# Optimization experiments

Measured on AMD Instinct MI355X. Metric: run time of the kernel, lower is better.

Reference implementation:

```python
import jax, jax.numpy as jnp
import numpy as np

ALPHA = 0.2  # leaky_relu negative slope


def setup_inputs() -> dict:
    key = jax.random.key(0)
    ks = jax.random.split(key, 6)
    N, E, F_IN, F_OUT, E_DIM = 50000, 800000, 256, 256, 64
    h = jax.random.normal(ks[0], (N, F_IN), dtype=jnp.float32)
    e_feat = jax.random.normal(ks[1], (E, E_DIM), dtype=jnp.float32)
    W = jax.random.normal(ks[2], (F_OUT, F_IN), dtype=jnp.float32) * (1.0 / np.sqrt(F_IN))
    A = jax.random.normal(ks[3], (1, 2 * F_OUT + E_DIM), dtype=jnp.float32) * 0.05
    src = jax.random.randint(ks[4], (E,), 0, N, dtype=jnp.int32)
    dst = jax.random.randint(ks[5], (E,), 0, N, dtype=jnp.int32)
    return {"h": h, "e_feat": e_feat, "W": W, "A": A, "src": src, "dst": dst}


def reference(h, e_feat, W, A, src, dst):
    N = h.shape[0]
    F_OUT = W.shape[0]
    # equation (1): node projection
    z = h @ W.T  # [N, F_OUT]
    z_src = z[src]  # [E, F_OUT]
    z_dst = z[dst]  # [E, F_OUT]
    # equation (2): per-edge attention logit = attn_fc([z_src, z_dst, e_feat])
    # split A to avoid materializing the [E, 2F+De] concat
    a_src, a_dst, a_e = A[0, :F_OUT], A[0, F_OUT:2 * F_OUT], A[0, 2 * F_OUT:]
    logits = z_src @ a_src + z_dst @ a_dst + e_feat @ a_e  # [E]
    e = jax.nn.leaky_relu(logits, ALPHA)
    # equations (3)&(4): segment-softmax over incoming edges per destination
    m = jax.ops.segment_max(e, dst, num_segments=N)  # [N]
    ex = jnp.exp(e - m[dst])
    denom = jax.ops.segment_sum(ex, dst, num_segments=N)  # [N]
    alpha = ex / denom[dst]  # [E]
    h_out = jax.ops.segment_sum(alpha[:, None] * z_src, dst, num_segments=N)
    return h_out
```

## Files before the change

### kernel.cpp

```cpp
#include <hip/hip_runtime.h>
#include <hip/hip_bf16.h>

#define FDIM 256
#define EDIM 64
#define LEAKY 0.2f

#define BM 128
#define BN 128
#define BK 32

typedef __attribute__((ext_vector_type(8))) short bfrag;
typedef __attribute__((ext_vector_type(4))) float f4acc;

__device__ __forceinline__ unsigned f2bf(float x){
    unsigned u = __float_as_uint(x);
    return (u + 0x7FFFu + ((u >> 16) & 1u)) >> 16;
}
__device__ __forceinline__ float bf2f(unsigned b){
    return __uint_as_float(b << 16);
}
__device__ __forceinline__ unsigned pack_hi(float x, float y, float& hx, float& hy){
    unsigned bx = f2bf(x), by = f2bf(y);
    hx = bf2f(bx); hy = bf2f(by);
    return bx | (by << 16);
}
__device__ __forceinline__ unsigned pack_lo(float rx, float ry){
    return f2bf(rx) | (f2bf(ry) << 16);
}

__global__ void k_init(float* __restrict__ s_src, float* __restrict__ s_dst,
                       int* __restrict__ counts, int N){
    int i = blockIdx.x*256 + threadIdx.x;
    if (i < N){ s_src[i] = 0.f; s_dst[i] = 0.f; counts[i] = 0; }
}

__global__ __launch_bounds__(256, 2) void k_gemm(const float* __restrict__ h,
                                                 const float* __restrict__ W,
                                                 const float* __restrict__ A,
                                                 unsigned short* __restrict__ z16,
                                                 float* __restrict__ s_src,
                                                 float* __restrict__ s_dst, int M){
    __shared__ uint4 smA[BM*8];
    __shared__ uint4 smB[BN*8];
    __shared__ float sred[2][2][BM];

    int tid = threadIdx.x;
    int m0 = blockIdx.x * BM;
    int n0 = blockIdx.y * BN;

    int wid  = tid >> 6;
    int lane = tid & 63;
    int wm = (wid >> 1) * 64;
    int wn = (wid & 1) * 64;
    int l15 = lane & 15;
    int l4  = lane >> 4;

    f4acc acc[4][4];
    #pragma unroll
    for (int i = 0; i < 4; ++i)
        #pragma unroll
        for (int j = 0; j < 4; ++j)
            acc[i][j] = (f4acc)(0.f);

    for (int kc = 0; kc < FDIM; kc += BK){
        #pragma unroll
        for (int q = 0; q < 4; ++q){
            int p = tid + q*256;
            int isB = p >= 512;
            int pp = p & 511;
            int row = pp >> 2, k8 = pp & 3;
            float4 v0, v1;
            if (isB){
                const float* g = &W[(n0 + row)*FDIM + kc + k8*8];
                v0 = *(const float4*)g; v1 = *(const float4*)(g + 4);
            } else {
                int gr = m0 + row;
                if (gr < M){
                    const float* g = &h[(size_t)gr*FDIM + kc + k8*8];
                    v0 = *(const float4*)g; v1 = *(const float4*)(g + 4);
                } else {
                    v0 = make_float4(0.f,0.f,0.f,0.f); v1 = v0;
                }
            }
            int sh = k8 ^ (row & 7);
            if (isB){
                uint4 hi; float hx, hy;
                hi.x = pack_hi(v0.x, v0.y, hx, hy);
                hi.y = pack_hi(v0.z, v0.w, hx, hy);
                hi.z = pack_hi(v1.x, v1.y, hx, hy);
                hi.w = pack_hi(v1.z, v1.w, hx, hy);
                smB[row*8 + sh] = hi;
            } else {
                uint4 hi, lo; float hx, hy;
                hi.x = pack_hi(v0.x, v0.y, hx, hy);
                lo.x = pack_lo(v0.x - hx, v0.y - hy);
                hi.y = pack_hi(v0.z, v0.w, hx, hy);
                lo.y = pack_lo(v0.z - hx, v0.w - hy);
                hi.z = pack_hi(v1.x, v1.y, hx, hy);
                lo.z = pack_lo(v1.x - hx, v1.y - hy);
                hi.w = pack_hi(v1.z, v1.w, hx, hy);
                lo.w = pack_lo(v1.z - hx, v1.w - hy);
                smA[row*8 + sh]       = hi;
                smA[row*8 + (sh ^ 4)] = lo;
            }
        }
        __syncthreads();

        bfrag ah[4], al[4];
        #pragma unroll
        for (int mf = 0; mf < 4; ++mf){
            int row = wm + mf*16 + l15;
            int sh = l4 ^ (row & 7);
            ah[mf] = *(const bfrag*)&smA[row*8 + sh];
            al[mf] = *(const bfrag*)&smA[row*8 + (sh ^ 4)];
        }
        #pragma unroll
        for (int nf = 0; nf < 4; ++nf){
            int row = wn + nf*16 + l15;
            int sh = l4 ^ (row & 7);
            bfrag bh = *(const bfrag*)&smB[row*8 + sh];
            #pragma unroll
            for (int mf = 0; mf < 4; ++mf){
                acc[mf][nf] = __builtin_amdgcn_mfma_f32_16x16x32_bf16(ah[mf], bh, acc[mf][nf], 0, 0, 0);
                acc[mf][nf] = __builtin_amdgcn_mfma_f32_16x16x32_bf16(al[mf], bh, acc[mf][nf], 0, 0, 0);
            }
        }
        __syncthreads();
    }

    #pragma unroll
    for (int mf = 0; mf < 4; ++mf){
        #pragma unroll
        for (int nf = 0; nf < 4; ++nf){
            int gcol = n0 + wn + nf*16 + l15;
            #pragma unroll
            for (int r = 0; r < 4; ++r){
                int grow = m0 + wm + mf*16 + l4*4 + r;
                if (grow < M)
                    z16[(size_t)grow*FDIM + gcol] = (unsigned short)f2bf(acc[mf][nf][r]);
            }
        }
    }

    float aS[4], aD[4];
    #pragma unroll
    for (int nf = 0; nf < 4; ++nf){
        int gcol = n0 + wn + nf*16 + l15;
        aS[nf] = A[gcol];
        aD[nf] = A[FDIM + gcol];
    }
    #pragma unroll
    for (int mf = 0; mf < 4; ++mf){
        #pragma unroll
        for (int r = 0; r < 4; ++r){
            float ps = 0.f, pd = 0.f;
            #pragma unroll
            for (int nf = 0; nf < 4; ++nf){
                ps += acc[mf][nf][r] * aS[nf];
                pd += acc[mf][nf][r] * aD[nf];
            }
            #pragma unroll
            for (int o = 1; o < 16; o <<= 1){
                ps += __shfl_xor(ps, o);
                pd += __shfl_xor(pd, o);
            }
            if (l15 == 0){
                int row = wm + mf*16 + l4*4 + r;
                sred[wid & 1][0][row] = ps;
                sred[wid & 1][1][row] = pd;
            }
        }
    }
    __syncthreads();
    if (tid < BM){
        int grow = m0 + tid;
        if (grow < M){
            atomicAdd(&s_src[grow], sred[0][0][tid] + sred[1][0][tid]);
            atomicAdd(&s_dst[grow], sred[0][1][tid] + sred[1][1][tid]);
        }
    }
}

__global__ void k_count(const int* __restrict__ dst, int* __restrict__ counts, int E){
    int e = blockIdx.x*256 + threadIdx.x;
    if (e < E) atomicAdd(&counts[dst[e]], 1);
}

__global__ void k_chunk_sums(const int* __restrict__ counts, int* __restrict__ bsums, int N){
    __shared__ int sh[256];
    int base = blockIdx.x*1024;
    int s = 0;
    for (int i = threadIdx.x; i < 1024; i += 256){
        int idx = base + i;
        s += (idx < N) ? counts[idx] : 0;
    }
    sh[threadIdx.x] = s; __syncthreads();
    for (int o = 128; o > 0; o >>= 1){
        if (threadIdx.x < o) sh[threadIdx.x] += sh[threadIdx.x + o];
        __syncthreads();
    }
    if (threadIdx.x == 0) bsums[blockIdx.x] = sh[0];
}

__global__ void k_scan_small(int* __restrict__ b, int nb){
    __shared__ int sh[1024];
    int tid = threadIdx.x;
    int v = (tid < nb) ? b[tid] : 0;
    sh[tid] = v; __syncthreads();
    int acc = v;
    for (int o = 1; o < 1024; o <<= 1){
        int t = (tid >= o) ? sh[tid - o] : 0;
        __syncthreads();
        acc += t; sh[tid] = acc;
        __syncthreads();
    }
    if (tid < nb) b[tid] = acc - v;
}

__global__ void k_scan_chunks(int* __restrict__ counts, int* __restrict__ cursor,
                              const int* __restrict__ bsums, int N, int E){
    __shared__ int sh[256];
    int tid = threadIdx.x;
    int base = blockIdx.x*1024 + tid*4;
    int v[4]; int s = 0;
    #pragma unroll
    for (int l = 0; l < 4; l++){
        int idx = base + l;
        v[l] = (idx < N) ? counts[idx] : 0;
        s += v[l];
    }
    sh[tid] = s; __syncthreads();
    int acc = s;
    for (int o = 1; o < 256; o <<= 1){
        int t = (tid >= o) ? sh[tid - o] : 0;
        __syncthreads();
        acc += t; sh[tid] = acc;
        __syncthreads();
    }
    int excl = acc - s + bsums[blockIdx.x];
    #pragma unroll
    for (int l = 0; l < 4; l++){
        int idx = base + l;
        if (idx < N){ counts[idx] = excl; cursor[idx] = excl; }
        excl += v[l];
    }
    if (blockIdx.x == 0 && tid == 0) counts[N] = E;
}

__global__ void k_edge(const float* __restrict__ ef, const float* __restrict__ A,
                       const float* __restrict__ s_src, const float* __restrict__ s_dst,
                       const int* __restrict__ src, const int* __restrict__ dst,
                       int* __restrict__ cursor, int2* __restrict__ epair, int E){
    int gt = blockIdx.x*256 + threadIdx.x;
    int e = gt >> 4, l4 = gt & 15;
    if (e >= E) return;
    float4 f  = *(const float4*)&ef[(size_t)e*EDIM + l4*4];
    float4 ae = *(const float4*)&A[2*FDIM + l4*4];
    float v = f.x*ae.x + f.y*ae.y + f.z*ae.z + f.w*ae.w;
    v += __shfl_xor(v, 8); v += __shfl_xor(v, 4);
    v += __shfl_xor(v, 2); v += __shfl_xor(v, 1);
    if (l4 == 0){
        int d = dst[e];
        float lg = v + s_src[src[e]] + s_dst[d];
        lg = lg > 0.f ? lg : LEAKY*lg;
        int p = atomicAdd(&cursor[d], 1);
        int2 pr; pr.x = src[e]; pr.y = __float_as_int(lg);
        epair[p] = pr;
    }
}

__global__ __launch_bounds__(256) void k_out(const unsigned short* __restrict__ z16,
                                             const int* __restrict__ offsets,
                                             const int2* __restrict__ epair,
                                             float* __restrict__ out, int N){
    int n = blockIdx.x*4 + (threadIdx.x >> 6);
    int lane = threadIdx.x & 63;
    if (n >= N) return;
    int i0 = offsets[n], i1 = offsets[n+1];

    float mlane = -3.402823466e38f;
    for (int i = i0 + lane; i < i1; i += 64)
        mlane = fmaxf(mlane, __int_as_float(epair[i].y));
    float mx = mlane;
    #pragma unroll
    for (int o = 32; o > 0; o >>= 1)
        mx = fmaxf(mx, __shfl_xor(mx, o));

    float4 a[4];
    a[0] = make_float4(0,0,0,0); a[1] = a[0]; a[2] = a[0]; a[3] = a[0];
    float dw = 0.f;
    const unsigned short* zb = z16 + lane*4;

    for (int base = i0; base < i1; base += 64){
        int cnt = min(64, i1 - base);
        int2 pe = make_int2(0, 0);
        float w = 0.f;
        if (lane < cnt){
            pe = epair[base + lane];
            w = __expf(__int_as_float(pe.y) - mx);
        }
        dw += w;
        int j = 0;
        for (; j + 7 < cnt; j += 8){
            float wj[8]; int sj[8]; uint2 rj[8];
            #pragma unroll
            for (int q = 0; q < 8; ++q){
                wj[q] = __shfl(w, j + q);
                sj[q] = __shfl(pe.x, j + q);
            }
            #pragma unroll
            for (int q = 0; q < 8; ++q)
                rj[q] = *(const uint2*)&zb[(size_t)sj[q]*FDIM];
            #pragma unroll
            for (int q = 0; q < 8; ++q){
                a[q & 3].x += wj[q]*bf2f(rj[q].x & 0xffffu);
                a[q & 3].y += wj[q]*bf2f(rj[q].x >> 16);
                a[q & 3].z += wj[q]*bf2f(rj[q].y & 0xffffu);
                a[q & 3].w += wj[q]*bf2f(rj[q].y >> 16);
            }
        }
        for (; j < cnt; ++j){
            float wq = __shfl(w, j);
            int   sq = __shfl(pe.x, j);
            uint2 r0 = *(const uint2*)&zb[(size_t)sq*FDIM];
            a[0].x += wq*bf2f(r0.x & 0xffffu);
            a[0].y += wq*bf2f(r0.x >> 16);
            a[0].z += wq*bf2f(r0.y & 0xffffu);
            a[0].w += wq*bf2f(r0.y >> 16);
        }
    }

    #pragma unroll
    for (int o = 32; o > 0; o >>= 1)
        dw += __shfl_xor(dw, o);

    float inv = (i1 > i0) ? 1.f / dw : 0.f;
    float4 res;
    res.x = ((a[0].x + a[1].x) + (a[2].x + a[3].x)) * inv;
    res.y = ((a[0].y + a[1].y) + (a[2].y + a[3].y)) * inv;
    res.z = ((a[0].z + a[1].z) + (a[2].z + a[3].z)) * inv;
    res.w = ((a[0].w + a[1].w) + (a[2].w + a[3].w)) * inv;
    *(float4*)&out[(size_t)n*FDIM + lane*4] = res;
}

extern "C" void kernel_launch(void* const* d_in, const int* in_sizes, int n_in,
                              void* d_out, int out_size, void* d_ws, size_t ws_size,
                              hipStream_t stream){
    const float* h  = (const float*)d_in[0];
    const float* ef = (const float*)d_in[1];
    const float* W  = (const float*)d_in[2];
    const float* A  = (const float*)d_in[3];
    const int*  src = (const int*)d_in[4];
    const int*  dst = (const int*)d_in[5];
    float* out = (float*)d_out;
    int N = in_sizes[0] / FDIM;
    int E = in_sizes[4];

    char* ws = (char*)d_ws;
    size_t off = 0;
    auto alloc = [&](size_t nbytes)->char*{
        char* p = ws + off;
        off = (off + nbytes + 255) & ~(size_t)255;
        return p;
    };
    unsigned short* z16 = (unsigned short*)alloc((size_t)N*FDIM*2);
    float* s_src  = (float*)alloc((size_t)N*4);
    float* s_dst  = (float*)alloc((size_t)N*4);
    int*   counts = (int*)alloc((size_t)(N+1)*4);
    int*   cursor = (int*)alloc((size_t)N*4);
    int2*  epair  = (int2*)alloc((size_t)E*8);
    int*   bsums  = (int*)alloc(1024*4);

    int nb = (N + 1023)/1024;

    hipLaunchKernelGGL(k_init, dim3((N+255)/256), dim3(256), 0, stream,
                       s_src, s_dst, counts, N);
    hipLaunchKernelGGL(k_gemm, dim3((N+BM-1)/BM, FDIM/BN), dim3(256), 0, stream,
                       h, W, A, z16, s_src, s_dst, N);
    hipLaunchKernelGGL(k_count, dim3((E+255)/256), dim3(256), 0, stream,
                       dst, counts, E);
    hipLaunchKernelGGL(k_chunk_sums, dim3(nb), dim3(256), 0, stream,
                       counts, bsums, N);
    hipLaunchKernelGGL(k_scan_small, dim3(1), dim3(1024), 0, stream,
                       bsums, nb);
    hipLaunchKernelGGL(k_scan_chunks, dim3(nb), dim3(256), 0, stream,
                       counts, cursor, bsums, N, E);
    hipLaunchKernelGGL(k_edge, dim3((E+15)/16), dim3(256), 0, stream,
                       ef, A, s_src, s_dst, src, dst, cursor, epair, E);
    hipLaunchKernelGGL(k_out, dim3((N+3)/4), dim3(256), 0, stream,
                       z16, counts, epair, out, N);
}
```

Baseline: 230.4 us.

## Widen GEMM tile to full output width and pre-convert W to bf16

The projection GEMM now covers all 256 output columns per block, so each h row tile is loaded and split into hi/lo bf16 once instead of twice. W is converted to bf16 once by a small kernel, and the atom-free direct stores of s_src/s_dst replace atomics; the init kernel becomes a memset of counts only. Cost: accumulator registers double (128 floats per thread), which may reduce occupancy or cause spills under launch_bounds(256,2), and the grid halves.

```diff
diff --git a/kernel.cpp b/kernel.cpp
--- a/kernel.cpp
+++ b/kernel.cpp
@@ -6,7 +6,7 @@
 #define LEAKY 0.2f
 
 #define BM 128
-#define BN 128
+#define BN 256
 #define BK 32
 
 typedef __attribute__((ext_vector_type(8))) short bfrag;
@@ -28,14 +28,17 @@
     return f2bf(rx) | (f2bf(ry) << 16);
 }
 
-__global__ void k_init(float* __restrict__ s_src, float* __restrict__ s_dst,
-                       int* __restrict__ counts, int N){
-    int i = blockIdx.x*256 + threadIdx.x;
-    if (i < N){ s_src[i] = 0.f; s_dst[i] = 0.f; counts[i] = 0; }
+__global__ void k_wconv(const float* __restrict__ W, unsigned short* __restrict__ W16){
+    int i = (blockIdx.x*256 + threadIdx.x) * 4;
+    float4 v = *(const float4*)&W[i];
+    uint2 o;
+    o.x = f2bf(v.x) | (f2bf(v.y) << 16);
+    o.y = f2bf(v.z) | (f2bf(v.w) << 16);
+    *(uint2*)&W16[i] = o;
 }
 
 __global__ __launch_bounds__(256, 2) void k_gemm(const float* __restrict__ h,
-                                                 const float* __restrict__ W,
+                                                 const unsigned short* __restrict__ W16,
                                                  const float* __restrict__ A,
                                                  unsigned short* __restrict__ z16,
                                                  float* __restrict__ s_src,
@@ -46,51 +49,35 @@
 
     int tid = threadIdx.x;
     int m0 = blockIdx.x * BM;
-    int n0 = blockIdx.y * BN;
 
     int wid  = tid >> 6;
     int lane = tid & 63;
     int wm = (wid >> 1) * 64;
-    int wn = (wid & 1) * 64;
+    int wn = (wid & 1) * 128;
     int l15 = lane & 15;
     int l4  = lane >> 4;
 
-    f4acc acc[4][4];
+    f4acc acc[4][8];
     #pragma unroll
     for (int i = 0; i < 4; ++i)
         #pragma unroll
-        for (int j = 0; j < 4; ++j)
+        for (int j = 0; j < 8; ++j)
             acc[i][j] = (f4acc)(0.f);
 
     for (int kc = 0; kc < FDIM; kc += BK){
         #pragma unroll
-        for (int q = 0; q < 4; ++q){
+        for (int q = 0; q < 6; ++q){
             int p = tid + q*256;
-            int isB = p >= 512;
-            int pp = p & 511;
-            int row = pp >> 2, k8 = pp & 3;
-            float4 v0, v1;
-            if (isB){
-                const float* g = &W[(n0 + row)*FDIM + kc + k8*8];
-                v0 = *(const float4*)g; v1 = *(const float4*)(g + 4);
-            } else {
+            if (p < 512){
+                int row = p >> 2, k8 = p & 3;
                 int gr = m0 + row;
+                float4 v0, v1;
                 if (gr < M){
                     const float* g = &h[(size_t)gr*FDIM + kc + k8*8];
                     v0 = *(const float4*)g; v1 = *(const float4*)(g + 4);
                 } else {
                     v0 = make_float4(0.f,0.f,0.f,0.f); v1 = v0;
                 }
-            }
-            int sh = k8 ^ (row & 7);
-            if (isB){
-                uint4 hi; float hx, hy;
-                hi.x = pack_hi(v0.x, v0.y, hx, hy);
-                hi.y = pack_hi(v0.z, v0.w, hx, hy);
-                hi.z = pack_hi(v1.x, v1.y, hx, hy);
-                hi.w = pack_hi(v1.z, v1.w, hx, hy);
-                smB[row*8 + sh] = hi;
-            } else {
                 uint4 hi, lo; float hx, hy;
                 hi.x = pack_hi(v0.x, v0.y, hx, hy);
                 lo.x = pack_lo(v0.x - hx, v0.y - hy);
@@ -100,8 +87,14 @@
                 lo.z = pack_lo(v1.x - hx, v1.y - hy);
                 hi.w = pack_hi(v1.z, v1.w, hx, hy);
                 lo.w = pack_lo(v1.z - hx, v1.w - hy);
+                int sh = k8 ^ (row & 7);
                 smA[row*8 + sh]       = hi;
                 smA[row*8 + (sh ^ 4)] = lo;
+            } else {
+                int pb = p - 512;
+                int row = pb >> 2, k8 = pb & 3;
+                uint4 v = *(const uint4*)&W16[(size_t)row*FDIM + kc + k8*8];
+                smB[row*8 + (k8 ^ (row & 7))] = v;
             }
         }
         __syncthreads();
@@ -115,10 +108,9 @@
             al[mf] = *(const bfrag*)&smA[row*8 + (sh ^ 4)];
         }
         #pragma unroll
-        for (int nf = 0; nf < 4; ++nf){
+        for (int nf = 0; nf < 8; ++nf){
             int row = wn + nf*16 + l15;
-            int sh = l4 ^ (row & 7);
-            bfrag bh = *(const bfrag*)&smB[row*8 + sh];
+            bfrag bh = *(const bfrag*)&smB[row*8 + (l4 ^ (row & 7))];
             #pragma unroll
             for (int mf = 0; mf < 4; ++mf){
                 acc[mf][nf] = __builtin_amdgcn_mfma_f32_16x16x32_bf16(ah[mf], bh, acc[mf][nf], 0, 0, 0);
@@ -131,8 +123,8 @@
     #pragma unroll
     for (int mf = 0; mf < 4; ++mf){
         #pragma unroll
-        for (int nf = 0; nf < 4; ++nf){
-            int gcol = n0 + wn + nf*16 + l15;
+        for (int nf = 0; nf < 8; ++nf){
+            int gcol = wn + nf*16 + l15;
             #pragma unroll
             for (int r = 0; r < 4; ++r){
                 int grow = m0 + wm + mf*16 + l4*4 + r;
@@ -142,10 +134,10 @@
         }
     }
 
-    float aS[4], aD[4];
-    #pragma unroll
-    for (int nf = 0; nf < 4; ++nf){
-        int gcol = n0 + wn + nf*16 + l15;
+    float aS[8], aD[8];
+    #pragma unroll
+    for (int nf = 0; nf < 8; ++nf){
+        int gcol = wn + nf*16 + l15;
         aS[nf] = A[gcol];
         aD[nf] = A[FDIM + gcol];
     }
@@ -155,7 +147,7 @@
         for (int r = 0; r < 4; ++r){
             float ps = 0.f, pd = 0.f;
             #pragma unroll
-            for (int nf = 0; nf < 4; ++nf){
+            for (int nf = 0; nf < 8; ++nf){
                 ps += acc[mf][nf][r] * aS[nf];
                 pd += acc[mf][nf][r] * aD[nf];
             }
@@ -175,8 +167,8 @@
     if (tid < BM){
         int grow = m0 + tid;
         if (grow < M){
-            atomicAdd(&s_src[grow], sred[0][0][tid] + sred[1][0][tid]);
-            atomicAdd(&s_dst[grow], sred[0][1][tid] + sred[1][1][tid]);
+            s_src[grow] = sred[0][0][tid] + sred[1][0][tid];
+            s_dst[grow] = sred[0][1][tid] + sred[1][1][tid];
         }
     }
 }
@@ -364,6 +356,7 @@
         return p;
     };
     unsigned short* z16 = (unsigned short*)alloc((size_t)N*FDIM*2);
+    unsigned short* W16 = (unsigned short*)alloc((size_t)FDIM*FDIM*2);
     float* s_src  = (float*)alloc((size_t)N*4);
     float* s_dst  = (float*)alloc((size_t)N*4);
     int*   counts = (int*)alloc((size_t)(N+1)*4);
@@ -373,10 +366,10 @@
 
     int nb = (N + 1023)/1024;
 
-    hipLaunchKernelGGL(k_init, dim3((N+255)/256), dim3(256), 0, stream,
-                       s_src, s_dst, counts, N);
-    hipLaunchKernelGGL(k_gemm, dim3((N+BM-1)/BM, FDIM/BN), dim3(256), 0, stream,
-                       h, W, A, z16, s_src, s_dst, N);
+    hipMemsetAsync(counts, 0, (size_t)(N+1)*4, stream);
+    hipLaunchKernelGGL(k_wconv, dim3(64), dim3(256), 0, stream, W, W16);
+    hipLaunchKernelGGL(k_gemm, dim3((N+BM-1)/BM), dim3(256), 0, stream,
+                       h, W16, A, z16, s_src, s_dst, N);
     hipLaunchKernelGGL(k_count, dim3((E+255)/256), dim3(256), 0, stream,
                        dst, counts, E);
     hipLaunchKernelGGL(k_chunk_sums, dim3(nb), dim3(256), 0, stream,
```

New measurement: 230.1 us, median of 2. Within noise of the previous version (-0.1%).
